# Performance work log

Hardware: AMD Instinct MI355X
Metric: run time of the kernel (lower is better)

## Reference

```python
import math
import jax, jax.numpy as jnp
import numpy as np

NUM_BUCKETS = 32
MAX_DISTANCE = 128
B, T, E, H, D = 2, 2048, 1024, 16, 64
INIT_SCALE = 0.1


def _relative_position_bucket(rel, num_buckets=NUM_BUCKETS, max_distance=MAX_DISTANCE):
    # T5-style bucketing; rel is int [T, T]
    nb = num_buckets // 2
    buckets = (rel > 0).astype(jnp.int32) * nb
    rel_abs = jnp.abs(rel)
    max_exact = nb // 2
    is_small = rel_abs < max_exact
    # guard log(0); those positions are selected by is_small anyway
    val_large = max_exact + (
        jnp.log(jnp.maximum(rel_abs, 1).astype(jnp.float32) / max_exact)
        / math.log(max_distance / max_exact) * (nb - max_exact)
    ).astype(jnp.int32)
    val_large = jnp.minimum(val_large, nb - 1)
    return buckets + jnp.where(is_small, rel_abs, val_large)


def setup_inputs() -> dict:
    key = jax.random.key(0)
    ks = jax.random.split(key, 6)
    x = jax.random.normal(ks[0], (B, T, E), dtype=jnp.float32)
    # nn.Linear weights are [out_features, in_features], init normal(std=0.1)
    Wq = jax.random.normal(ks[1], (H * D, E), dtype=jnp.float32) * INIT_SCALE
    Wk = jax.random.normal(ks[2], (H * D, E), dtype=jnp.float32) * INIT_SCALE
    Wv = jax.random.normal(ks[3], (H * D, E), dtype=jnp.float32) * INIT_SCALE
    Wo = jax.random.normal(ks[4], (E, H * D), dtype=jnp.float32) * INIT_SCALE
    # nn.Embedding default init: standard normal
    rel_emb = jax.random.normal(ks[5], (NUM_BUCKETS, H), dtype=jnp.float32)
    return {"x": x, "Wq": Wq, "Wk": Wk, "Wv": Wv, "Wo": Wo, "rel_emb": rel_emb}


def reference(x, Wq, Wk, Wv, Wo, rel_emb):
    b, t, _ = x.shape
    scale = D ** (-0.5)
    q = jnp.einsum('bte,fe->btf', x, Wq).reshape(b, t, H, D).transpose(0, 2, 1, 3)
    k = jnp.einsum('bte,fe->btf', x, Wk).reshape(b, t, H, D).transpose(0, 2, 1, 3)
    v = jnp.einsum('bte,fe->btf', x, Wv).reshape(b, t, H, D).transpose(0, 2, 1, 3)
    attn = jnp.einsum('bhtd,bhsd->bhts', q, k) * scale  # [B,H,T,T]
    # T5 relative position bias
    pos = jnp.arange(t)
    rel = pos[:, None] - pos[None, :]
    buckets = _relative_position_bucket(rel)
    bias = rel_emb[buckets]                    # [T,T,H]
    attn = attn + bias.transpose(2, 0, 1)[None]  # [1,H,T,T]
    # causal mask (triu, diagonal=1)
    causal = jnp.triu(jnp.ones((t, t), dtype=bool), k=1)
    attn = jnp.where(causal[None, None], -jnp.inf, attn)
    attn = jax.nn.softmax(attn, axis=-1)
    out = jnp.einsum('bhts,bhsd->bhtd', attn, v).transpose(0, 2, 1, 3).reshape(b, t, H * D)
    return jnp.einsum('btf,ef->bte', out, Wo)
```

## Files before the change

kernel.cpp:

```cpp
#include <hip/hip_runtime.h>
#include <hip/hip_bf16.h>
#include <stdint.h>


typedef __attribute__((ext_vector_type(8))) short bf16x8;
typedef __attribute__((ext_vector_type(4))) float f32x4;

#define MFMA16(a, b, c) __builtin_amdgcn_mfma_f32_16x16x32_bf16((a), (b), (c), 0, 0, 0)

typedef __attribute__((address_space(1))) void gvoid_t;
typedef __attribute__((address_space(3))) void lvoid_t;

__device__ __forceinline__ void gload16(const void* g, void* l) {
    __builtin_amdgcn_global_load_lds((gvoid_t*)g, (lvoid_t*)l, 16, 0, 0);
}

__device__ __forceinline__ ushort f2bf_rne(float f) {
    union { float f; uint32_t u; } v; v.f = f;
    uint32_t u = v.u;
    return (ushort)((u + 0x7FFFu + ((u >> 16) & 1u)) >> 16);
}

__global__ void cvt_f2bf(const float* __restrict__ in, ushort* __restrict__ out, int n) {
    int i = (blockIdx.x * 256 + threadIdx.x) * 4;
    if (i + 3 < n) {
        float4 f = *(const float4*)(in + i);
        ushort4 o;
        o.x = f2bf_rne(f.x); o.y = f2bf_rne(f.y);
        o.z = f2bf_rne(f.z); o.w = f2bf_rne(f.w);
        *(ushort4*)(out + i) = o;
    }
}

__global__ void build_bias(const float* __restrict__ rel_emb, float* __restrict__ bias_tab) {
    int idx = blockIdx.x * 256 + threadIdx.x;
    int h = idx >> 11, rel = idx & 2047;
    int bucket;
    if (rel == 0) bucket = 0;
    else if (rel < 8) bucket = 16 + rel;
    else {
        int t;
        if      (rel >= 91) t = 7;
        else if (rel >= 64) t = 6;
        else if (rel >= 46) t = 5;
        else if (rel >= 32) t = 4;
        else if (rel >= 23) t = 3;
        else if (rel >= 16) t = 2;
        else if (rel >= 12) t = 1;
        else                t = 0;
        bucket = 24 + t;
    }
    bias_tab[idx] = rel_emb[bucket * 16 + h];
}

template<int MODE>
__global__ __launch_bounds__(256, 2) void gemm_bt(
    const ushort* __restrict__ A,
    const ushort* __restrict__ W0, const ushort* __restrict__ W1, const ushort* __restrict__ W2,
    ushort* __restrict__ outq, ushort* __restrict__ outk, ushort* __restrict__ outvt,
    float* __restrict__ outf)
{
    __shared__ __align__(16) ushort lsA[128 * 32];
    __shared__ __align__(16) ushort lsB[128 * 32];
    const int tid = threadIdx.x;
    const int lane = tid & 63, w = tid >> 6;
    const int g = lane >> 4, c16 = lane & 15;
    const int m0 = blockIdx.x * 128;
    const int wm = w >> 1, wn = w & 1;

    const ushort* W;
    int n0, widx = 0;
    if (MODE == 0) {
        widx = blockIdx.y >> 3;
        W = (widx == 0) ? W0 : (widx == 1) ? W1 : W2;
        n0 = (blockIdx.y & 7) * 128;
    } else {
        W = W0;
        n0 = blockIdx.y * 128;
    }

    f32x4 acc[4][4];
    #pragma unroll
    for (int i = 0; i < 4; i++)
        #pragma unroll
        for (int j = 0; j < 4; j++) acc[i][j] = (f32x4){0.f, 0.f, 0.f, 0.f};

    int crow[2], cj[2];
    #pragma unroll
    for (int i = 0; i < 2; i++) {
        int c = (i * 4 + w) * 64 + lane;
        crow[i] = c >> 2;
        cj[i] = (c & 3) ^ ((crow[i] >> 1) & 3);
    }

    for (int kt = 0; kt < 1024; kt += 32) {
        #pragma unroll
        for (int i = 0; i < 2; i++) {
            gload16(A + (m0 + crow[i]) * 1024 + kt + cj[i] * 8, lsA + (i * 4 + w) * 512);
            gload16(W + (n0 + crow[i]) * 1024 + kt + cj[i] * 8, lsB + (i * 4 + w) * 512);
        }
        __syncthreads();
        bf16x8 af[4], bf[4];
        #pragma unroll
        for (int mi = 0; mi < 4; mi++) {
            int row = wm * 64 + mi * 16 + c16;
            af[mi] = *(const bf16x8*)(lsA + row * 32 + ((g ^ ((row >> 1) & 3)) * 8));
        }
        #pragma unroll
        for (int ni = 0; ni < 4; ni++) {
            int row = wn * 64 + ni * 16 + c16;
            bf[ni] = *(const bf16x8*)(lsB + row * 32 + ((g ^ ((row >> 1) & 3)) * 8));
        }
        #pragma unroll
        for (int mi = 0; mi < 4; mi++)
            #pragma unroll
            for (int ni = 0; ni < 4; ni++)
                acc[mi][ni] = MFMA16(af[mi], bf[ni], acc[mi][ni]);
        __syncthreads();
    }

    #pragma unroll
    for (int mi = 0; mi < 4; mi++) {
        #pragma unroll
        for (int ni = 0; ni < 4; ni++) {
            int mg = m0 + wm * 64 + mi * 16 + g * 4;
            if (MODE == 0) {
                int f = n0 + wn * 64 + ni * 16 + c16;
                int h = f >> 6, d = f & 63;
                if (widx < 2) {
                    ushort* dst = (widx == 0) ? outq : outk;
                    #pragma unroll
                    for (int r = 0; r < 4; r++) {
                        int m = mg + r, b = m >> 11, t = m & 2047;
                        dst[((b * 16 + h) * 2048 + t) * 64 + d] = f2bf_rne(acc[mi][ni][r]);
                    }
                } else {
                    int b = mg >> 11, t = mg & 2047;
                    ushort4 pk;
                    pk.x = f2bf_rne(acc[mi][ni][0]); pk.y = f2bf_rne(acc[mi][ni][1]);
                    pk.z = f2bf_rne(acc[mi][ni][2]); pk.w = f2bf_rne(acc[mi][ni][3]);
                    *(ushort4*)(outvt + ((size_t)(b * 16 + h) * 64 + d) * 2048 + t) = pk;
                }
            } else {
                int ng = n0 + wn * 64 + ni * 16 + c16;
                #pragma unroll
                for (int r = 0; r < 4; r++) {
                    int m = mg + r;
                    outf[(size_t)m * 1024 + ng] = acc[mi][ni][r];
                }
            }
        }
    }
}

__global__ __launch_bounds__(256, 2) void attn_kernel(
    const ushort* __restrict__ qb_, const ushort* __restrict__ kb_,
    const ushort* __restrict__ vtb, const float* __restrict__ bias_tab,
    ushort* __restrict__ ob)
{
    __shared__ __align__(16) ushort Qs[64 * 64];
    __shared__ __align__(16) ushort Ks[64 * 64];
    __shared__ __align__(16) ushort Vs[64 * 64];
    __shared__ __align__(16) ushort Ps[4][16 * 72];

    const int tid = threadIdx.x, lane = tid & 63, w = tid >> 6;
    const int g = lane >> 4, c16 = lane & 15;
    const int bh = blockIdx.y;
    const int qb = (blockIdx.x + bh) & 31;
    const int b = bh >> 4, h = bh & 15;

    const ushort* qh = qb_ + (size_t)bh * 2048 * 64;
    const ushort* kh = kb_ + (size_t)bh * 2048 * 64;
    const ushort* vh = vtb + (size_t)bh * 64 * 2048;
    const float* bt = bias_tab + h * 2048;
    const int q0 = qb * 64;

    int crow[2], cj[2];
    #pragma unroll
    for (int i = 0; i < 2; i++) {
        int c = (i * 4 + w) * 64 + lane;
        crow[i] = c >> 3;
        cj[i] = (c & 7) ^ (crow[i] & 7);
    }

    #pragma unroll
    for (int i = 0; i < 2; i++)
        gload16(qh + (q0 + crow[i]) * 64 + cj[i] * 8, Qs + (i * 4 + w) * 512);
    __syncthreads();

    bf16x8 qf[2];
    {
        int row = w * 16 + c16;
        #pragma unroll
        for (int kk = 0; kk < 2; kk++)
            qf[kk] = *(const bf16x8*)(Qs + row * 64 + (((kk * 4 + g) ^ (row & 7)) * 8));
    }
    const int qrow = q0 + w * 16 + c16;

    float m_run = -1e30f, l_run = 0.f;
    f32x4 o[4];
    #pragma unroll
    for (int ni = 0; ni < 4; ni++) o[ni] = (f32x4){0.f, 0.f, 0.f, 0.f};
    const float bias_far = bt[128];

    for (int j64 = 0; j64 <= qb; j64++) {
        const int k0 = j64 * 64;
        __syncthreads();
        #pragma unroll
        for (int i = 0; i < 2; i++) {
            gload16(kh + (k0 + crow[i]) * 64 + cj[i] * 8, Ks + (i * 4 + w) * 512);
            gload16(vh + crow[i] * 2048 + k0 + cj[i] * 8, Vs + (i * 4 + w) * 512);
        }
        __syncthreads();

        f32x4 s[4];
        #pragma unroll
        for (int f = 0; f < 4; f++) s[f] = (f32x4){0.f, 0.f, 0.f, 0.f};
        #pragma unroll
        for (int kk = 0; kk < 2; kk++) {
            #pragma unroll
            for (int f = 0; f < 4; f++) {
                int row = f * 16 + c16;
                bf16x8 a = *(const bf16x8*)(Ks + row * 64 + (((kk * 4 + g) ^ (row & 7)) * 8));
                s[f] = MFMA16(a, qf[kk], s[f]);
            }
        }

        const bool near = (qb - j64) < 3;
        const bool diag = (j64 == qb);
        float p[4][4];
        float mt = -1e30f;
        #pragma unroll
        for (int f = 0; f < 4; f++) {
            #pragma unroll
            for (int r = 0; r < 4; r++) {
                int kpos = k0 + f * 16 + g * 4 + r;
                int rel = qrow - kpos;
                float lg;
                if (diag && rel < 0) lg = -1e30f;
                else {
                    float bias = near ? bt[rel] : bias_far;
                    lg = s[f][r] * 0.125f + bias;
                }
                p[f][r] = lg;
                mt = fmaxf(mt, lg);
            }
        }
        mt = fmaxf(mt, __shfl_xor(mt, 16));
        mt = fmaxf(mt, __shfl_xor(mt, 32));
        float m_new = fmaxf(m_run, mt);
        float alpha = __expf(m_run - m_new);
        float lt = 0.f;
        #pragma unroll
        for (int f = 0; f < 4; f++)
            #pragma unroll
            for (int r = 0; r < 4; r++) {
                float e = __expf(p[f][r] - m_new);
                p[f][r] = e;
                lt += e;
            }
        lt += __shfl_xor(lt, 16);
        lt += __shfl_xor(lt, 32);
        l_run = l_run * alpha + lt;
        m_run = m_new;
        #pragma unroll
        for (int ni = 0; ni < 4; ni++) {
            o[ni][0] *= alpha; o[ni][1] *= alpha; o[ni][2] *= alpha; o[ni][3] *= alpha;
        }

        #pragma unroll
        for (int f = 0; f < 4; f++) {
            ushort4 pk;
            pk.x = f2bf_rne(p[f][0]); pk.y = f2bf_rne(p[f][1]);
            pk.z = f2bf_rne(p[f][2]); pk.w = f2bf_rne(p[f][3]);
            *(ushort4*)(&Ps[w][c16 * 72 + f * 16 + g * 4]) = pk;
        }
        #pragma unroll
        for (int kk = 0; kk < 2; kk++) {
            bf16x8 pf = *(const bf16x8*)(&Ps[w][c16 * 72 + kk * 32 + g * 8]);
            #pragma unroll
            for (int ni = 0; ni < 4; ni++) {
                int row = ni * 16 + c16;
                bf16x8 av = *(const bf16x8*)(Vs + row * 64 + (((kk * 4 + g) ^ (row & 7)) * 8));
                o[ni] = MFMA16(av, pf, o[ni]);
            }
        }
    }

    float inv = 1.f / l_run;
    size_t base = ((size_t)(b * 2048 + qrow)) * 1024 + h * 64;
    #pragma unroll
    for (int ni = 0; ni < 4; ni++) {
        ushort4 pk;
        pk.x = f2bf_rne(o[ni][0] * inv); pk.y = f2bf_rne(o[ni][1] * inv);
        pk.z = f2bf_rne(o[ni][2] * inv); pk.w = f2bf_rne(o[ni][3] * inv);
        *(ushort4*)(ob + base + ni * 16 + g * 4) = pk;
    }
}

extern "C" void kernel_launch(void* const* d_in, const int* in_sizes, int n_in,
                              void* d_out, int out_size, void* d_ws, size_t ws_size,
                              hipStream_t stream) {
    const float* x       = (const float*)d_in[0];
    const float* Wq      = (const float*)d_in[1];
    const float* Wk      = (const float*)d_in[2];
    const float* Wv      = (const float*)d_in[3];
    const float* Wo      = (const float*)d_in[4];
    const float* rel_emb = (const float*)d_in[5];

    char* ws = (char*)d_ws;
    ushort* xbf = (ushort*)(ws);
    ushort* wqb = (ushort*)(ws + (8u  << 20));
    ushort* wkb = (ushort*)(ws + (10u << 20));
    ushort* wvb = (ushort*)(ws + (12u << 20));
    ushort* wob = (ushort*)(ws + (14u << 20));
    ushort* qbf = (ushort*)(ws + (16u << 20));
    ushort* kbf = (ushort*)(ws + (24u << 20));
    ushort* vtb = (ushort*)(ws + (32u << 20));
    ushort* obf = (ushort*)(ws + (40u << 20));
    float*  btab = (float*)(ws + (48u << 20));

    cvt_f2bf<<<4096, 256, 0, stream>>>(x,  xbf, 4194304);
    cvt_f2bf<<<1024, 256, 0, stream>>>(Wq, wqb, 1048576);
    cvt_f2bf<<<1024, 256, 0, stream>>>(Wk, wkb, 1048576);
    cvt_f2bf<<<1024, 256, 0, stream>>>(Wv, wvb, 1048576);
    cvt_f2bf<<<1024, 256, 0, stream>>>(Wo, wob, 1048576);
    build_bias<<<128, 256, 0, stream>>>(rel_emb, btab);

    gemm_bt<0><<<dim3(32, 24), 256, 0, stream>>>(xbf, wqb, wkb, wvb, qbf, kbf, vtb, nullptr);
    attn_kernel<<<dim3(32, 32), 256, 0, stream>>>(qbf, kbf, vtb, btab, obf);
    gemm_bt<1><<<dim3(32, 8), 256, 0, stream>>>(obf, wob, nullptr, nullptr,
                                                nullptr, nullptr, nullptr, (float*)d_out);
}
```

Baseline: 203.0 us.

## Double-buffer GEMM and attention LDS tiles, merge conversion launches, retune occupancy

New measurement: 210.7 us. +3.8%, slower.

```diff
diff --git a/kernel.cpp b/kernel.cpp
--- a/kernel.cpp
+++ b/kernel.cpp
@@ -21,15 +21,23 @@
     return (ushort)((u + 0x7FFFu + ((u >> 16) & 1u)) >> 16);
 }
 
-__global__ void cvt_f2bf(const float* __restrict__ in, ushort* __restrict__ out, int n) {
+__global__ void cvt_all(const float* __restrict__ x,
+                        const float* __restrict__ wq, const float* __restrict__ wk,
+                        const float* __restrict__ wv, const float* __restrict__ wo,
+                        ushort* __restrict__ out) {
     int i = (blockIdx.x * 256 + threadIdx.x) * 4;
-    if (i + 3 < n) {
-        float4 f = *(const float4*)(in + i);
-        ushort4 o;
-        o.x = f2bf_rne(f.x); o.y = f2bf_rne(f.y);
-        o.z = f2bf_rne(f.z); o.w = f2bf_rne(f.w);
-        *(ushort4*)(out + i) = o;
-    }
+    int sel = i >> 20;
+    const float* src; int off;
+    if (sel < 4) { src = x; off = i; }
+    else {
+        src = (sel == 4) ? wq : (sel == 5) ? wk : (sel == 6) ? wv : wo;
+        off = i & 1048575;
+    }
+    float4 f = *(const float4*)(src + off);
+    ushort4 o;
+    o.x = f2bf_rne(f.x); o.y = f2bf_rne(f.y);
+    o.z = f2bf_rne(f.z); o.w = f2bf_rne(f.w);
+    *(ushort4*)(out + i) = o;
 }
 
 __global__ void build_bias(const float* __restrict__ rel_emb, float* __restrict__ bias_tab) {
@@ -54,18 +62,21 @@
 }
 
 template<int MODE>
-__global__ __launch_bounds__(256, 2) void gemm_bt(
+__global__ __launch_bounds__(256, MODE == 0 ? 3 : 4) void gemm_bt(
     const ushort* __restrict__ A,
     const ushort* __restrict__ W0, const ushort* __restrict__ W1, const ushort* __restrict__ W2,
     ushort* __restrict__ outq, ushort* __restrict__ outk, ushort* __restrict__ outvt,
     float* __restrict__ outf)
 {
-    __shared__ __align__(16) ushort lsA[128 * 32];
-    __shared__ __align__(16) ushort lsB[128 * 32];
+    constexpr int BM  = (MODE == 0) ? 128 : 64;
+    constexpr int ACH = BM / 64;
+    constexpr int MI  = (MODE == 0) ? 4 : 2;
+    __shared__ __align__(16) ushort lsA[2][BM * 32];
+    __shared__ __align__(16) ushort lsB[2][128 * 32];
     const int tid = threadIdx.x;
     const int lane = tid & 63, w = tid >> 6;
     const int g = lane >> 4, c16 = lane & 15;
-    const int m0 = blockIdx.x * 128;
+    const int m0 = blockIdx.x * BM;
     const int wm = w >> 1, wn = w & 1;
 
     const ushort* W;
@@ -79,51 +90,65 @@
         n0 = blockIdx.y * 128;
     }
 
-    f32x4 acc[4][4];
-    #pragma unroll
-    for (int i = 0; i < 4; i++)
+    f32x4 acc[MI][4];
+    #pragma unroll
+    for (int i = 0; i < MI; i++)
         #pragma unroll
         for (int j = 0; j < 4; j++) acc[i][j] = (f32x4){0.f, 0.f, 0.f, 0.f};
 
-    int crow[2], cj[2];
+    int acrow[ACH], acj[ACH], bcrow[2], bcj[2];
+    #pragma unroll
+    for (int i = 0; i < ACH; i++) {
+        int c = (i * 4 + w) * 64 + lane;
+        acrow[i] = c >> 2; acj[i] = (c & 3) ^ ((acrow[i] >> 1) & 3);
+    }
     #pragma unroll
     for (int i = 0; i < 2; i++) {
         int c = (i * 4 + w) * 64 + lane;
-        crow[i] = c >> 2;
-        cj[i] = (c & 3) ^ ((crow[i] >> 1) & 3);
-    }
-
-    for (int kt = 0; kt < 1024; kt += 32) {
-        #pragma unroll
-        for (int i = 0; i < 2; i++) {
-            gload16(A + (m0 + crow[i]) * 1024 + kt + cj[i] * 8, lsA + (i * 4 + w) * 512);
-            gload16(W + (n0 + crow[i]) * 1024 + kt + cj[i] * 8, lsB + (i * 4 + w) * 512);
-        }
-        __syncthreads();
-        bf16x8 af[4], bf[4];
-        #pragma unroll
-        for (int mi = 0; mi < 4; mi++) {
-            int row = wm * 64 + mi * 16 + c16;
-            af[mi] = *(const bf16x8*)(lsA + row * 32 + ((g ^ ((row >> 1) & 3)) * 8));
+        bcrow[i] = c >> 2; bcj[i] = (c & 3) ^ ((bcrow[i] >> 1) & 3);
+    }
+
+    auto stage = [&](int buf, int kt) {
+        #pragma unroll
+        for (int i = 0; i < ACH; i++)
+            gload16(A + (size_t)(m0 + acrow[i]) * 1024 + kt + acj[i] * 8,
+                    &lsA[buf][(i * 4 + w) * 512]);
+        #pragma unroll
+        for (int i = 0; i < 2; i++)
+            gload16(W + (size_t)(n0 + bcrow[i]) * 1024 + kt + bcj[i] * 8,
+                    &lsB[buf][(i * 4 + w) * 512]);
+    };
+
+    stage(0, 0);
+    __syncthreads();
+
+    for (int it = 0; it < 32; ++it) {
+        const int cur = it & 1;
+        if (it < 31) stage(cur ^ 1, (it + 1) * 32);
+        bf16x8 af[MI], bfv[4];
+        #pragma unroll
+        for (int mi = 0; mi < MI; mi++) {
+            int row = wm * (16 * MI) + mi * 16 + c16;
+            af[mi] = *(const bf16x8*)(&lsA[cur][row * 32 + ((g ^ ((row >> 1) & 3)) * 8)]);
         }
         #pragma unroll
         for (int ni = 0; ni < 4; ni++) {
             int row = wn * 64 + ni * 16 + c16;
-            bf[ni] = *(const bf16x8*)(lsB + row * 32 + ((g ^ ((row >> 1) & 3)) * 8));
-        }
-        #pragma unroll
-        for (int mi = 0; mi < 4; mi++)
+            bfv[ni] = *(const bf16x8*)(&lsB[cur][row * 32 + ((g ^ ((row >> 1) & 3)) * 8)]);
+        }
+        #pragma unroll
+        for (int mi = 0; mi < MI; mi++)
             #pragma unroll
             for (int ni = 0; ni < 4; ni++)
-                acc[mi][ni] = MFMA16(af[mi], bf[ni], acc[mi][ni]);
+                acc[mi][ni] = MFMA16(af[mi], bfv[ni], acc[mi][ni]);
         __syncthreads();
     }
 
     #pragma unroll
-    for (int mi = 0; mi < 4; mi++) {
+    for (int mi = 0; mi < MI; mi++) {
         #pragma unroll
         for (int ni = 0; ni < 4; ni++) {
-            int mg = m0 + wm * 64 + mi * 16 + g * 4;
+            int mg = m0 + wm * (16 * MI) + mi * 16 + g * 4;
             if (MODE == 0) {
                 int f = n0 + wn * 64 + ni * 16 + c16;
                 int h = f >> 6, d = f & 63;
@@ -153,14 +178,12 @@
     }
 }
 
-__global__ __launch_bounds__(256, 2) void attn_kernel(
+__global__ __launch_bounds__(256, 3) void attn_kernel(
     const ushort* __restrict__ qb_, const ushort* __restrict__ kb_,
     const ushort* __restrict__ vtb, const float* __restrict__ bias_tab,
     ushort* __restrict__ ob)
 {
-    __shared__ __align__(16) ushort Qs[64 * 64];
-    __shared__ __align__(16) ushort Ks[64 * 64];
-    __shared__ __align__(16) ushort Vs[64 * 64];
+    __shared__ __align__(16) ushort KV[2][2][4096];
     __shared__ __align__(16) ushort Ps[4][16 * 72];
 
     const int tid = threadIdx.x, lane = tid & 63, w = tid >> 6;
@@ -183,19 +206,23 @@
         cj[i] = (c & 7) ^ (crow[i] & 7);
     }
 
-    #pragma unroll
-    for (int i = 0; i < 2; i++)
-        gload16(qh + (q0 + crow[i]) * 64 + cj[i] * 8, Qs + (i * 4 + w) * 512);
+    auto stageKV = [&](int buf, int j64) {
+        int k0 = j64 * 64;
+        #pragma unroll
+        for (int i = 0; i < 2; i++) {
+            gload16(kh + (size_t)(k0 + crow[i]) * 64 + cj[i] * 8, &KV[buf][0][(i * 4 + w) * 512]);
+            gload16(vh + (size_t)crow[i] * 2048 + k0 + cj[i] * 8, &KV[buf][1][(i * 4 + w) * 512]);
+        }
+    };
+
+    const int qrow = q0 + w * 16 + c16;
+    bf16x8 qf[2];
+    #pragma unroll
+    for (int kk = 0; kk < 2; kk++)
+        qf[kk] = *(const bf16x8*)(qh + (size_t)qrow * 64 + kk * 32 + g * 8);
+
+    stageKV(0, 0);
     __syncthreads();
-
-    bf16x8 qf[2];
-    {
-        int row = w * 16 + c16;
-        #pragma unroll
-        for (int kk = 0; kk < 2; kk++)
-            qf[kk] = *(const bf16x8*)(Qs + row * 64 + (((kk * 4 + g) ^ (row & 7)) * 8));
-    }
-    const int qrow = q0 + w * 16 + c16;
 
     float m_run = -1e30f, l_run = 0.f;
     f32x4 o[4];
@@ -204,18 +231,16 @@
     const float bias_far = bt[128];
 
     for (int j64 = 0; j64 <= qb; j64++) {
+        const int cur = j64 & 1;
+        if (j64 < qb) stageKV(cur ^ 1, j64 + 1);
+        const ushort* Ks = KV[cur][0];
+        const ushort* Vs = KV[cur][1];
         const int k0 = j64 * 64;
-        __syncthreads();
-        #pragma unroll
-        for (int i = 0; i < 2; i++) {
-            gload16(kh + (k0 + crow[i]) * 64 + cj[i] * 8, Ks + (i * 4 + w) * 512);
-            gload16(vh + crow[i] * 2048 + k0 + cj[i] * 8, Vs + (i * 4 + w) * 512);
-        }
-        __syncthreads();
 
         f32x4 s[4];
         #pragma unroll
         for (int f = 0; f < 4; f++) s[f] = (f32x4){0.f, 0.f, 0.f, 0.f};
+        __builtin_amdgcn_s_setprio(1);
         #pragma unroll
         for (int kk = 0; kk < 2; kk++) {
             #pragma unroll
@@ -225,6 +250,7 @@
                 s[f] = MFMA16(a, qf[kk], s[f]);
             }
         }
+        __builtin_amdgcn_s_setprio(0);
 
         const bool near = (qb - j64) < 3;
         const bool diag = (j64 == qb);
@@ -275,6 +301,7 @@
             pk.z = f2bf_rne(p[f][2]); pk.w = f2bf_rne(p[f][3]);
             *(ushort4*)(&Ps[w][c16 * 72 + f * 16 + g * 4]) = pk;
         }
+        __builtin_amdgcn_s_setprio(1);
         #pragma unroll
         for (int kk = 0; kk < 2; kk++) {
             bf16x8 pf = *(const bf16x8*)(&Ps[w][c16 * 72 + kk * 32 + g * 8]);
@@ -285,6 +312,8 @@
                 o[ni] = MFMA16(av, pf, o[ni]);
             }
         }
+        __builtin_amdgcn_s_setprio(0);
+        __syncthreads();
     }
 
     float inv = 1.f / l_run;
@@ -320,15 +349,11 @@
     ushort* obf = (ushort*)(ws + (40u << 20));
     float*  btab = (float*)(ws + (48u << 20));
 
-    cvt_f2bf<<<4096, 256, 0, stream>>>(x,  xbf, 4194304);
-    cvt_f2bf<<<1024, 256, 0, stream>>>(Wq, wqb, 1048576);
-    cvt_f2bf<<<1024, 256, 0, stream>>>(Wk, wkb, 1048576);
-    cvt_f2bf<<<1024, 256, 0, stream>>>(Wv, wvb, 1048576);
-    cvt_f2bf<<<1024, 256, 0, stream>>>(Wo, wob, 1048576);
+    cvt_all<<<8192, 256, 0, stream>>>(x, Wq, Wk, Wv, Wo, xbf);
     build_bias<<<128, 256, 0, stream>>>(rel_emb, btab);
 
     gemm_bt<0><<<dim3(32, 24), 256, 0, stream>>>(xbf, wqb, wkb, wvb, qbf, kbf, vtb, nullptr);
     attn_kernel<<<dim3(32, 32), 256, 0, stream>>>(qbf, kbf, vtb, btab, obf);
-    gemm_bt<1><<<dim3(32, 8), 256, 0, stream>>>(obf, wob, nullptr, nullptr,
+    gemm_bt<1><<<dim3(64, 8), 256, 0, stream>>>(obf, wob, nullptr, nullptr,
                                                 nullptr, nullptr, nullptr, (float*)d_out);
 }
```
